# Performance work log

Hardware: AMD Instinct MI355X
Metric: run time of the kernel (lower is better)

Reference implementation:

```python
import jax, jax.numpy as jnp
import numpy as np

N_NODES = 50000

def setup_inputs() -> dict:
    key = jax.random.key(0)
    ks = jax.random.split(key, 8)
    d_in, d_h = 128, 128
    x = jax.random.normal(ks[0], (N_NODES, d_in), dtype=jnp.float32)
    edge_index = jax.random.randint(ks[1], (2, 800000), 0, N_NODES, dtype=jnp.int64)
    edge_pairs = jax.random.randint(ks[2], (1000000, 2), 0, N_NODES, dtype=jnp.int64)
    W_gcn = jax.random.normal(ks[3], (d_in, d_h), dtype=jnp.float32) / np.sqrt(d_in)
    b_gcn = jnp.zeros((d_h,), dtype=jnp.float32)
    W1 = jax.random.normal(ks[4], (2 * d_h, d_h), dtype=jnp.float32) / np.sqrt(2 * d_h)
    b1 = jnp.zeros((d_h,), dtype=jnp.float32)
    W2 = jax.random.normal(ks[5], (d_h, 1), dtype=jnp.float32) / np.sqrt(d_h)
    b2 = jnp.zeros((1,), dtype=jnp.float32)
    return {"x": x, "edge_index": edge_index, "edge_pairs": edge_pairs,
            "W_gcn": W_gcn, "b_gcn": b_gcn, "W1": W1, "b1": b1, "W2": W2, "b2": b2}

def gcn_conv(x, edge_index, W, b):
    # PyG GCNConv default: add self-loops, symmetric normalization.
    n = x.shape[0]
    loop = jnp.arange(n, dtype=edge_index.dtype)
    src = jnp.concatenate([edge_index[0], loop])  # [E+N]
    dst = jnp.concatenate([edge_index[1], loop])
    deg = jax.ops.segment_sum(jnp.ones(src.shape[0], dtype=x.dtype), dst, num_segments=n)
    dinv = jnp.where(deg > 0, jax.lax.rsqrt(deg), 0.0)
    norm = dinv[src] * dinv[dst]                  # [E+N]
    h = x @ W                                     # [N, H]
    agg = jax.ops.segment_sum(h[src] * norm[:, None], dst, num_segments=n)
    return agg + b

def reference(x, edge_index, edge_pairs, W_gcn, b_gcn, W1, b1, W2, b2):
    h = gcn_conv(x, edge_index, W_gcn, b_gcn)      # [N, H]
    e = jnp.concatenate([h[edge_pairs[:, 0]], h[edge_pairs[:, 1]]], axis=-1)  # [P, 2H]
    edge_logits = jax.nn.relu(e @ W1 + b1) @ W2 + b2  # [P, 1]
    return edge_logits, edge_pairs, h
```

## Files before the change

kernel.cpp:

```cpp
#include <hip/hip_runtime.h>
#include <hip/hip_fp16.h>

#define WG 256

typedef _Float16 f16;
typedef _Float16 hv2 __attribute__((ext_vector_type(2)));
typedef _Float16 f16x4 __attribute__((ext_vector_type(4)));
typedef _Float16 f16x8 __attribute__((ext_vector_type(8)));
typedef float f32x4 __attribute__((ext_vector_type(4)));

__global__ __launch_bounds__(WG) void k_deg_count(const int* __restrict__ dst,
                                                  int* __restrict__ deg,
                                                  int* __restrict__ rank, int e) {
    int i = blockIdx.x * WG + threadIdx.x;
    if (i < e) rank[i] = atomicAdd(&deg[dst[i]], 1);
}

__global__ __launch_bounds__(WG) void k_scan1(const int* __restrict__ deg,
                                              float* __restrict__ dinv,
                                              int* __restrict__ base,
                                              int* __restrict__ bsum, int n) {
    __shared__ int t[WG];
    int tid = threadIdx.x;
    int i = blockIdx.x * WG + tid;
    int v = (i < n) ? deg[i] : 0;
    if (i < n) dinv[i] = rsqrtf((float)(v + 1));
    t[tid] = v;
    __syncthreads();
    for (int o = 1; o < WG; o <<= 1) {
        int add = (tid >= o) ? t[tid - o] : 0;
        __syncthreads();
        t[tid] += add;
        __syncthreads();
    }
    if (i < n) base[i] = t[tid] - v;
    if (tid == WG - 1) bsum[blockIdx.x] = t[WG - 1];
}

__global__ __launch_bounds__(WG) void k_scan23(int* __restrict__ base,
                                               const int* __restrict__ bsum,
                                               int n, int e, int nb) {
    __shared__ int t[WG];
    int tid = threadIdx.x;
    int v = (tid < nb) ? bsum[tid] : 0;
    t[tid] = v;
    __syncthreads();
    for (int o = 1; o < WG; o <<= 1) {
        int add = (tid >= o) ? t[tid - o] : 0;
        __syncthreads();
        t[tid] += add;
        __syncthreads();
    }
    int off = t[blockIdx.x] - ((blockIdx.x < nb) ? bsum[blockIdx.x] : 0);
    int i = blockIdx.x * WG + tid;
    if (i < n) {
        base[i] += off;
        if (i == n - 1) base[n] = e;
    }
}

__global__ __launch_bounds__(WG) void k_fill(const int* __restrict__ src,
                                             const int* __restrict__ dst,
                                             const int* __restrict__ base,
                                             const int* __restrict__ rank,
                                             int* __restrict__ esrc, int e) {
    int i = blockIdx.x * WG + threadIdx.x;
    if (i >= e) return;
    esrc[base[dst[i]] + rank[i]] = src[i];
}

__global__ __launch_bounds__(WG) void k_misc(const float* __restrict__ Wg,
                                             f16* __restrict__ Wgt,
                                             const float* __restrict__ W1,
                                             f16* __restrict__ W1t,
                                             const int* __restrict__ pairs,
                                             float* __restrict__ outp, int n4) {
    int b = blockIdx.x;
    if (b < 64) {
        int i = b * WG + threadIdx.x;
        int k = i & 127, nI = i >> 7;
        Wgt[i] = (f16)Wg[(size_t)k * 128 + nI];
    } else if (b < 192) {
        int i = (b - 64) * WG + threadIdx.x;
        int k = i & 255, nI = i >> 8;
        W1t[i] = (f16)W1[(size_t)k * 128 + nI];
    } else {
        int i = (b - 192) * WG + threadIdx.x;
        if (i < n4) {
            int4 v = ((const int4*)pairs)[i];
            ((float4*)outp)[i] = make_float4((float)v.x, (float)v.y, (float)v.z, (float)v.w);
        }
    }
}

__global__ __launch_bounds__(WG) void k_mm_hpk(const float* __restrict__ A,
                                               const f16* __restrict__ Wt,
                                               const float* __restrict__ dinv,
                                               __half2* __restrict__ Out, int n) {
    __shared__ f16 As[64][136];
    __shared__ f16 Bs[128][136];
    const int tid = threadIdx.x;
    const int row0 = blockIdx.x * 64;
    for (int f = tid; f < 128 * 16; f += WG) {
        int r = f >> 4, c = f & 15;
        *(float4*)&Bs[r][c * 8] = ((const float4*)Wt)[r * 16 + c];
    }
    for (int f = tid; f < 64 * 32; f += WG) {
        int r = f >> 5, c = f & 31;
        float4 v = make_float4(0.f, 0.f, 0.f, 0.f);
        if (row0 + r < n) v = ((const float4*)A)[(size_t)(row0 + r) * 32 + c];
        *(f16x4*)&As[r][c * 4] = (f16x4){(f16)v.x, (f16)v.y, (f16)v.z, (f16)v.w};
    }
    __syncthreads();
    const int wv = tid >> 6, lane = tid & 63, m = lane & 15, quad = lane >> 4;
    f32x4 acc[8];
#pragma unroll
    for (int t = 0; t < 8; ++t) acc[t] = (f32x4){0.f, 0.f, 0.f, 0.f};
#pragma unroll
    for (int kk = 0; kk < 4; ++kk) {
        f16x8 af = *(f16x8*)&As[wv * 16 + m][kk * 32 + quad * 8];
#pragma unroll
        for (int t = 0; t < 8; ++t) {
            f16x8 bf = *(f16x8*)&Bs[t * 16 + m][kk * 32 + quad * 8];
            acc[t] = __builtin_amdgcn_mfma_f32_16x16x32_f16(af, bf, acc[t], 0, 0, 0);
        }
    }
#pragma unroll
    for (int r = 0; r < 4; ++r) {
        int row = row0 + wv * 16 + quad * 4 + r;
        if (row < n) {
            float dv = dinv[row];
#pragma unroll
            for (int t = 0; t < 4; ++t)
                Out[(size_t)row * 64 + t * 16 + m] =
                    __floats2half2_rn(acc[t][r] * dv, acc[t + 4][r] * dv);
        }
    }
}

__global__ __launch_bounds__(WG) void k_mm_uv(const float* __restrict__ A,
                                              const f16* __restrict__ W1t,
                                              const float* __restrict__ b1,
                                              __half2* __restrict__ Up,
                                              __half2* __restrict__ Vp, int n) {
    __shared__ f16 As[64][136];
    __shared__ f16 Bs[128][136];
    const int tid = threadIdx.x;
    const int row0 = blockIdx.x * 64;
    for (int f = tid; f < 64 * 32; f += WG) {
        int r = f >> 5, c = f & 31;
        float4 v = make_float4(0.f, 0.f, 0.f, 0.f);
        if (row0 + r < n) v = ((const float4*)A)[(size_t)(row0 + r) * 32 + c];
        *(f16x4*)&As[r][c * 4] = (f16x4){(f16)v.x, (f16)v.y, (f16)v.z, (f16)v.w};
    }
    const int wv = tid >> 6, lane = tid & 63, m = lane & 15, quad = lane >> 4;
    f32x4 acc[8];
#pragma unroll
    for (int ph = 0; ph < 2; ++ph) {
        if (ph) __syncthreads();
        for (int f = tid; f < 128 * 16; f += WG) {
            int r = f >> 4, c = f & 15;
            *(float4*)&Bs[r][c * 8] = *(const float4*)(W1t + (size_t)r * 256 + ph * 128 + c * 8);
        }
        __syncthreads();
#pragma unroll
        for (int t = 0; t < 8; ++t) acc[t] = (f32x4){0.f, 0.f, 0.f, 0.f};
#pragma unroll
        for (int kk = 0; kk < 4; ++kk) {
            f16x8 af = *(f16x8*)&As[wv * 16 + m][kk * 32 + quad * 8];
#pragma unroll
            for (int t = 0; t < 8; ++t) {
                f16x8 bf = *(f16x8*)&Bs[t * 16 + m][kk * 32 + quad * 8];
                acc[t] = __builtin_amdgcn_mfma_f32_16x16x32_f16(af, bf, acc[t], 0, 0, 0);
            }
        }
        __half2* Out = ph ? Vp : Up;
#pragma unroll
        for (int t = 0; t < 4; ++t) {
            float bl = 0.f, bh = 0.f;
            if (!ph) { bl = b1[t * 16 + m]; bh = b1[t * 16 + m + 64]; }
#pragma unroll
            for (int r = 0; r < 4; ++r) {
                int row = row0 + wv * 16 + quad * 4 + r;
                if (row < n)
                    Out[(size_t)row * 64 + t * 16 + m] =
                        __floats2half2_rn(acc[t][r] + bl, acc[t + 4][r] + bh);
            }
        }
    }
}

__global__ __launch_bounds__(WG) void k_gather(const __half2* __restrict__ Hpk,
                                               const float* __restrict__ dinv,
                                               const float* __restrict__ bg,
                                               const int* __restrict__ base,
                                               const int* __restrict__ esrc,
                                               float* __restrict__ outh, int n) {
    int tid = threadIdx.x;
    int node = blockIdx.x * 16 + (tid >> 4);
    int sub = tid & 15;
    if (node >= n) return;
    int4 hh = *(const int4*)(Hpk + (size_t)node * 64 + 4 * sub);
    const int* hp = (const int*)&hh;
    float accl[4], acch[4];
#pragma unroll
    for (int k = 0; k < 4; ++k) {
        hv2 h = __builtin_bit_cast(hv2, hp[k]);
        accl[k] = (float)h[0];
        acch[k] = (float)h[1];
    }
    int j = base[node], jend = base[node + 1];
    for (; j + 4 <= jend; j += 4) {
        int s0 = esrc[j], s1 = esrc[j + 1], s2i = esrc[j + 2], s3 = esrc[j + 3];
        int4 r0 = *(const int4*)(Hpk + (size_t)s0 * 64 + 4 * sub);
        int4 r1 = *(const int4*)(Hpk + (size_t)s1 * 64 + 4 * sub);
        int4 r2 = *(const int4*)(Hpk + (size_t)s2i * 64 + 4 * sub);
        int4 r3 = *(const int4*)(Hpk + (size_t)s3 * 64 + 4 * sub);
        const int* p0 = (const int*)&r0;
        const int* p1 = (const int*)&r1;
        const int* p2 = (const int*)&r2;
        const int* p3 = (const int*)&r3;
#pragma unroll
        for (int k = 0; k < 4; ++k) {
            hv2 h0 = __builtin_bit_cast(hv2, p0[k]);
            hv2 h1 = __builtin_bit_cast(hv2, p1[k]);
            hv2 h2 = __builtin_bit_cast(hv2, p2[k]);
            hv2 h3 = __builtin_bit_cast(hv2, p3[k]);
            accl[k] += (float)h0[0] + (float)h1[0] + (float)h2[0] + (float)h3[0];
            acch[k] += (float)h0[1] + (float)h1[1] + (float)h2[1] + (float)h3[1];
        }
    }
    for (; j < jend; ++j) {
        int s = esrc[j];
        int4 r = *(const int4*)(Hpk + (size_t)s * 64 + 4 * sub);
        const int* pr = (const int*)&r;
#pragma unroll
        for (int k = 0; k < 4; ++k) {
            hv2 h = __builtin_bit_cast(hv2, pr[k]);
            accl[k] += (float)h[0];
            acch[k] += (float)h[1];
        }
    }
    float dv = dinv[node];
    float4 blo = *(const float4*)(bg + 4 * sub);
    float4 bhi = *(const float4*)(bg + 4 * sub + 64);
    *(float4*)&outh[(size_t)node * 128 + 4 * sub] =
        make_float4(fmaf(accl[0], dv, blo.x), fmaf(accl[1], dv, blo.y),
                    fmaf(accl[2], dv, blo.z), fmaf(accl[3], dv, blo.w));
    *(float4*)&outh[(size_t)node * 128 + 64 + 4 * sub] =
        make_float4(fmaf(acch[0], dv, bhi.x), fmaf(acch[1], dv, bhi.y),
                    fmaf(acch[2], dv, bhi.z), fmaf(acch[3], dv, bhi.w));
}

__global__ __launch_bounds__(WG) void k_pair16(const __half2* __restrict__ U,
                                               const __half2* __restrict__ V,
                                               const float* __restrict__ W2,
                                               const float* __restrict__ b2,
                                               const int* __restrict__ pairs,
                                               float* __restrict__ out_logit, int p) {
    int wv = (blockIdx.x * WG + threadIdx.x) >> 6;
    int lane = threadIdx.x & 63;
    int g = lane >> 4, sub = lane & 15;
    int qb = wv * 16 + g;
    if (qb >= p) return;
    int q0 = qb;
    int q1 = (qb + 4 < p) ? qb + 4 : qb;
    int q2 = (qb + 8 < p) ? qb + 8 : qb;
    int q3 = (qb + 12 < p) ? qb + 12 : qb;
    int a0 = pairs[2 * q0], b0 = pairs[2 * q0 + 1];
    int a1 = pairs[2 * q1], b1i = pairs[2 * q1 + 1];
    int a2 = pairs[2 * q2], b2i = pairs[2 * q2 + 1];
    int a3 = pairs[2 * q3], b3i = pairs[2 * q3 + 1];

    int4 u0 = *(const int4*)(U + (size_t)a0 * 64 + 4 * sub);
    int4 v0 = *(const int4*)(V + (size_t)b0 * 64 + 4 * sub);
    int4 u1 = *(const int4*)(U + (size_t)a1 * 64 + 4 * sub);
    int4 v1 = *(const int4*)(V + (size_t)b1i * 64 + 4 * sub);
    int4 u2 = *(const int4*)(U + (size_t)a2 * 64 + 4 * sub);
    int4 v2 = *(const int4*)(V + (size_t)b2i * 64 + 4 * sub);
    int4 u3 = *(const int4*)(U + (size_t)a3 * 64 + 4 * sub);
    int4 v3 = *(const int4*)(V + (size_t)b3i * 64 + 4 * sub);

    float4 w2lo = ((const float4*)W2)[sub];
    float4 w2hi = ((const float4*)(W2 + 64))[sub];
    hv2 w2h[4];
    w2h[0] = hv2{(f16)w2lo.x, (f16)w2hi.x};
    w2h[1] = hv2{(f16)w2lo.y, (f16)w2hi.y};
    w2h[2] = hv2{(f16)w2lo.z, (f16)w2hi.z};
    w2h[3] = hv2{(f16)w2lo.w, (f16)w2hi.w};

    const int* ui0 = (const int*)&u0;
    const int* vi0 = (const int*)&v0;
    const int* ui1 = (const int*)&u1;
    const int* vi1 = (const int*)&v1;
    const int* ui2 = (const int*)&u2;
    const int* vi2 = (const int*)&v2;
    const int* ui3 = (const int*)&u3;
    const int* vi3 = (const int*)&v3;

    const hv2 z2 = hv2{(f16)0.f, (f16)0.f};
    float p0 = 0.f, p1 = 0.f, p2 = 0.f, p3 = 0.f;
#pragma unroll
    for (int k = 0; k < 4; ++k) {
        hv2 s0 = __builtin_bit_cast(hv2, ui0[k]) + __builtin_bit_cast(hv2, vi0[k]);
        hv2 s1 = __builtin_bit_cast(hv2, ui1[k]) + __builtin_bit_cast(hv2, vi1[k]);
        hv2 s2 = __builtin_bit_cast(hv2, ui2[k]) + __builtin_bit_cast(hv2, vi2[k]);
        hv2 s3 = __builtin_bit_cast(hv2, ui3[k]) + __builtin_bit_cast(hv2, vi3[k]);
        p0 = __builtin_amdgcn_fdot2(__builtin_elementwise_max(s0, z2), w2h[k], p0, false);
        p1 = __builtin_amdgcn_fdot2(__builtin_elementwise_max(s1, z2), w2h[k], p1, false);
        p2 = __builtin_amdgcn_fdot2(__builtin_elementwise_max(s2, z2), w2h[k], p2, false);
        p3 = __builtin_amdgcn_fdot2(__builtin_elementwise_max(s3, z2), w2h[k], p3, false);
    }
#pragma unroll
    for (int m = 1; m < 16; m <<= 1) {
        p0 += __shfl_xor(p0, m, 64);
        p1 += __shfl_xor(p1, m, 64);
        p2 += __shfl_xor(p2, m, 64);
        p3 += __shfl_xor(p3, m, 64);
    }
    if (sub == 0) {
        float bb = b2[0];
        out_logit[q0] = p0 + bb;
        if (qb + 4 < p) out_logit[qb + 4] = p1 + bb;
        if (qb + 8 < p) out_logit[qb + 8] = p2 + bb;
        if (qb + 12 < p) out_logit[qb + 12] = p3 + bb;
    }
}

extern "C" void kernel_launch(void* const* d_in, const int* in_sizes, int n_in,
                              void* d_out, int out_size, void* d_ws, size_t ws_size,
                              hipStream_t stream) {
    const float* x     = (const float*)d_in[0];
    const int*   eidx  = (const int*)d_in[1];
    const int*   pairs = (const int*)d_in[2];
    const float* W_gcn = (const float*)d_in[3];
    const float* b_gcn = (const float*)d_in[4];
    const float* W1    = (const float*)d_in[5];
    const float* b1    = (const float*)d_in[6];
    const float* W2    = (const float*)d_in[7];
    const float* b2    = (const float*)d_in[8];

    const int N = in_sizes[0] / 128;
    const int E = in_sizes[1] / 2;
    const int P = in_sizes[2] / 2;
    const int* esrc_in = eidx;
    const int* edst_in = eidx + E;

    float* ws      = (float*)d_ws;
    int*   deg     = (int*)d_ws;
    float* dinv    = ws + 65536;
    int*   base    = (int*)(ws + 131072);
    int*   bsum    = (int*)(ws + 196608);
    f16*   Wt_gcn  = (f16*)(ws + 197120);
    f16*   W1t     = (f16*)(ws + 205312);
    int*   rank    = (int*)(ws + 221696);
    int*   ecsr    = (int*)(ws + 221696 + (size_t)E);
    __half2* Hpk   = (__half2*)(ws + 221696 + 2 * (size_t)E);
    __half2* Upk   = Hpk + (size_t)N * 64;
    __half2* Vpk   = Upk + (size_t)N * 64;

    float* out_logit = (float*)d_out;
    float* out_pairs = out_logit + P;
    float* out_h     = out_logit + 3 * (size_t)P;

    const int nb = (N + WG - 1) / WG;
    dim3 blk(WG);
    dim3 grid_pair((unsigned)((P + 63) / 64));
    dim3 grid_misc((unsigned)(192 + (P / 2 + WG - 1) / WG));
    hipMemsetAsync(deg, 0, (size_t)N * 4, stream);
    k_deg_count <<<(E + WG - 1) / WG, blk, 0, stream>>>(edst_in, deg, rank, E);
    k_scan1     <<<nb, blk, 0, stream>>>(deg, dinv, base, bsum, N);
    k_scan23    <<<nb, blk, 0, stream>>>(base, bsum, N, E, nb);
    k_fill      <<<(E + WG - 1) / WG, blk, 0, stream>>>(esrc_in, edst_in, base, rank, ecsr, E);
    k_misc      <<<grid_misc, blk, 0, stream>>>(W_gcn, Wt_gcn, W1, W1t, pairs, out_pairs, P / 2);
    k_mm_hpk    <<<(N + 63) / 64, blk, 0, stream>>>(x, Wt_gcn, dinv, Hpk, N);
    k_gather    <<<(N + 15) / 16, blk, 0, stream>>>(Hpk, dinv, b_gcn, base, ecsr, out_h, N);
    k_mm_uv     <<<(N + 63) / 64, blk, 0, stream>>>(out_h, W1t, b1, Upk, Vpk, N);
    k_pair16    <<<grid_pair, blk, 0, stream>>>(Upk, Vpk, W2, b2, pairs, out_logit, P);
}
```

Baseline: 276.6 us.

## Fuse degree counting, pair conversion and X@W GEMM into one interleaved launch

The dinv prescale is moved out of the GEMM epilogue and into the gather, where each neighbor's row is scaled by its own dinv through FMAs. The GEMM therefore no longer depends on the degree count. That lets the degree atomics, the pair int-to-float conversion and the X@W GEMM run as interleaved block slots of a single launch. The goal is to overlap the atomic-bound and bandwidth-bound work with the MFMA GEMM and to drop one launch. In exchange, the gather does an extra dinv lookup per edge, and the grid carries idle blocks wherever the slot counts differ.

```diff
diff --git a/kernel.cpp b/kernel.cpp
--- a/kernel.cpp
+++ b/kernel.cpp
@@ -9,11 +9,88 @@
 typedef _Float16 f16x8 __attribute__((ext_vector_type(8)));
 typedef float f32x4 __attribute__((ext_vector_type(4)));
 
-__global__ __launch_bounds__(WG) void k_deg_count(const int* __restrict__ dst,
-                                                  int* __restrict__ deg,
-                                                  int* __restrict__ rank, int e) {
-    int i = blockIdx.x * WG + threadIdx.x;
-    if (i < e) rank[i] = atomicAdd(&deg[dst[i]], 1);
+__global__ __launch_bounds__(WG) void k_misc0(const float* __restrict__ Wg,
+                                              f16* __restrict__ Wgt,
+                                              const float* __restrict__ W1,
+                                              f16* __restrict__ W1t) {
+    int b = blockIdx.x;
+    if (b < 64) {
+        int i = b * WG + threadIdx.x;
+        int k = i & 127, nI = i >> 7;
+        Wgt[i] = (f16)Wg[(size_t)k * 128 + nI];
+    } else {
+        int i = (b - 64) * WG + threadIdx.x;
+        int k = i & 255, nI = i >> 8;
+        W1t[i] = (f16)W1[(size_t)k * 128 + nI];
+    }
+}
+
+__global__ __launch_bounds__(WG) void k_fusedA(const float* __restrict__ A,
+                                               const f16* __restrict__ Wt,
+                                               __half2* __restrict__ Out, int n,
+                                               const int* __restrict__ dst,
+                                               int* __restrict__ deg,
+                                               int* __restrict__ rank, int e,
+                                               const int* __restrict__ pairs,
+                                               float* __restrict__ outp, int n4,
+                                               int nmm, int necnt, int ncvt) {
+    __shared__ __align__(16) char smem[64 * 136 * 2 + 128 * 136 * 2];
+    int b = blockIdx.x, slot = b & 3, idx = b >> 2;
+    int tid = threadIdx.x;
+    if (slot == 1 || slot == 3) {
+        int hid = idx * 2 + (slot >> 1);
+        if (hid >= necnt) return;
+        int i = hid * WG + tid;
+        if (i < e) rank[i] = atomicAdd(&deg[dst[i]], 1);
+        return;
+    }
+    if (slot == 2) {
+        if (idx >= ncvt) return;
+        int i = idx * WG + tid;
+        if (i < n4) {
+            int4 v = ((const int4*)pairs)[i];
+            ((float4*)outp)[i] = make_float4((float)v.x, (float)v.y, (float)v.z, (float)v.w);
+        }
+        return;
+    }
+    if (idx >= nmm) return;
+    f16(*As)[136] = (f16(*)[136])smem;
+    f16(*Bs)[136] = (f16(*)[136])(smem + 64 * 136 * 2);
+    const int row0 = idx * 64;
+    for (int f = tid; f < 128 * 16; f += WG) {
+        int r = f >> 4, c = f & 15;
+        *(float4*)&Bs[r][c * 8] = ((const float4*)Wt)[r * 16 + c];
+    }
+    for (int f = tid; f < 64 * 32; f += WG) {
+        int r = f >> 5, c = f & 31;
+        float4 v = make_float4(0.f, 0.f, 0.f, 0.f);
+        if (row0 + r < n) v = ((const float4*)A)[(size_t)(row0 + r) * 32 + c];
+        *(f16x4*)&As[r][c * 4] = (f16x4){(f16)v.x, (f16)v.y, (f16)v.z, (f16)v.w};
+    }
+    __syncthreads();
+    const int wv = tid >> 6, lane = tid & 63, m = lane & 15, quad = lane >> 4;
+    f32x4 acc[8];
+#pragma unroll
+    for (int t = 0; t < 8; ++t) acc[t] = (f32x4){0.f, 0.f, 0.f, 0.f};
+#pragma unroll
+    for (int kk = 0; kk < 4; ++kk) {
+        f16x8 af = *(f16x8*)&As[wv * 16 + m][kk * 32 + quad * 8];
+#pragma unroll
+        for (int t = 0; t < 8; ++t) {
+            f16x8 bf = *(f16x8*)&Bs[t * 16 + m][kk * 32 + quad * 8];
+            acc[t] = __builtin_amdgcn_mfma_f32_16x16x32_f16(af, bf, acc[t], 0, 0, 0);
+        }
+    }
+#pragma unroll
+    for (int r = 0; r < 4; ++r) {
+        int row = row0 + wv * 16 + quad * 4 + r;
+        if (row < n) {
+#pragma unroll
+            for (int t = 0; t < 4; ++t)
+                Out[(size_t)row * 64 + t * 16 + m] =
+                    __floats2half2_rn(acc[t][r], acc[t + 4][r]);
+        }
+    }
 }
 
 __global__ __launch_bounds__(WG) void k_scan1(const int* __restrict__ deg,
@@ -69,73 +146,74 @@
     esrc[base[dst[i]] + rank[i]] = src[i];
 }
 
-__global__ __launch_bounds__(WG) void k_misc(const float* __restrict__ Wg,
-                                             f16* __restrict__ Wgt,
-                                             const float* __restrict__ W1,
-                                             f16* __restrict__ W1t,
-                                             const int* __restrict__ pairs,
-                                             float* __restrict__ outp, int n4) {
-    int b = blockIdx.x;
-    if (b < 64) {
-        int i = b * WG + threadIdx.x;
-        int k = i & 127, nI = i >> 7;
-        Wgt[i] = (f16)Wg[(size_t)k * 128 + nI];
-    } else if (b < 192) {
-        int i = (b - 64) * WG + threadIdx.x;
-        int k = i & 255, nI = i >> 8;
-        W1t[i] = (f16)W1[(size_t)k * 128 + nI];
-    } else {
-        int i = (b - 192) * WG + threadIdx.x;
-        if (i < n4) {
-            int4 v = ((const int4*)pairs)[i];
-            ((float4*)outp)[i] = make_float4((float)v.x, (float)v.y, (float)v.z, (float)v.w);
-        }
-    }
-}
-
-__global__ __launch_bounds__(WG) void k_mm_hpk(const float* __restrict__ A,
-                                               const f16* __restrict__ Wt,
+__global__ __launch_bounds__(WG) void k_gather(const __half2* __restrict__ Hpk,
                                                const float* __restrict__ dinv,
-                                               __half2* __restrict__ Out, int n) {
-    __shared__ f16 As[64][136];
-    __shared__ f16 Bs[128][136];
-    const int tid = threadIdx.x;
-    const int row0 = blockIdx.x * 64;
-    for (int f = tid; f < 128 * 16; f += WG) {
-        int r = f >> 4, c = f & 15;
-        *(float4*)&Bs[r][c * 8] = ((const float4*)Wt)[r * 16 + c];
-    }
-    for (int f = tid; f < 64 * 32; f += WG) {
-        int r = f >> 5, c = f & 31;
-        float4 v = make_float4(0.f, 0.f, 0.f, 0.f);
-        if (row0 + r < n) v = ((const float4*)A)[(size_t)(row0 + r) * 32 + c];
-        *(f16x4*)&As[r][c * 4] = (f16x4){(f16)v.x, (f16)v.y, (f16)v.z, (f16)v.w};
-    }
-    __syncthreads();
-    const int wv = tid >> 6, lane = tid & 63, m = lane & 15, quad = lane >> 4;
-    f32x4 acc[8];
-#pragma unroll
-    for (int t = 0; t < 8; ++t) acc[t] = (f32x4){0.f, 0.f, 0.f, 0.f};
-#pragma unroll
-    for (int kk = 0; kk < 4; ++kk) {
-        f16x8 af = *(f16x8*)&As[wv * 16 + m][kk * 32 + quad * 8];
-#pragma unroll
-        for (int t = 0; t < 8; ++t) {
-            f16x8 bf = *(f16x8*)&Bs[t * 16 + m][kk * 32 + quad * 8];
-            acc[t] = __builtin_amdgcn_mfma_f32_16x16x32_f16(af, bf, acc[t], 0, 0, 0);
-        }
-    }
-#pragma unroll
-    for (int r = 0; r < 4; ++r) {
-        int row = row0 + wv * 16 + quad * 4 + r;
-        if (row < n) {
-            float dv = dinv[row];
-#pragma unroll
-            for (int t = 0; t < 4; ++t)
-                Out[(size_t)row * 64 + t * 16 + m] =
-                    __floats2half2_rn(acc[t][r] * dv, acc[t + 4][r] * dv);
-        }
-    }
+                                               const float* __restrict__ bg,
+                                               const int* __restrict__ base,
+                                               const int* __restrict__ esrc,
+                                               float* __restrict__ outh, int n) {
+    int tid = threadIdx.x;
+    int node = blockIdx.x * 16 + (tid >> 4);
+    int sub = tid & 15;
+    if (node >= n) return;
+    float dv = dinv[node];
+    int4 hh = *(const int4*)(Hpk + (size_t)node * 64 + 4 * sub);
+    const int* hp = (const int*)&hh;
+    float accl[4], acch[4];
+#pragma unroll
+    for (int k = 0; k < 4; ++k) {
+        hv2 h = __builtin_bit_cast(hv2, hp[k]);
+        accl[k] = (float)h[0] * dv;
+        acch[k] = (float)h[1] * dv;
+    }
+    int j = base[node], jend = base[node + 1];
+    for (; j + 4 <= jend; j += 4) {
+        int s0 = esrc[j], s1 = esrc[j + 1], s2i = esrc[j + 2], s3 = esrc[j + 3];
+        float ds0 = dinv[s0], ds1 = dinv[s1], ds2 = dinv[s2i], ds3 = dinv[s3];
+        int4 r0 = *(const int4*)(Hpk + (size_t)s0 * 64 + 4 * sub);
+        int4 r1 = *(const int4*)(Hpk + (size_t)s1 * 64 + 4 * sub);
+        int4 r2 = *(const int4*)(Hpk + (size_t)s2i * 64 + 4 * sub);
+        int4 r3 = *(const int4*)(Hpk + (size_t)s3 * 64 + 4 * sub);
+        const int* p0 = (const int*)&r0;
+        const int* p1 = (const int*)&r1;
+        const int* p2 = (const int*)&r2;
+        const int* p3 = (const int*)&r3;
+#pragma unroll
+        for (int k = 0; k < 4; ++k) {
+            hv2 h0 = __builtin_bit_cast(hv2, p0[k]);
+            hv2 h1 = __builtin_bit_cast(hv2, p1[k]);
+            hv2 h2 = __builtin_bit_cast(hv2, p2[k]);
+            hv2 h3 = __builtin_bit_cast(hv2, p3[k]);
+            accl[k] = fmaf((float)h0[0], ds0, accl[k]);
+            accl[k] = fmaf((float)h1[0], ds1, accl[k]);
+            accl[k] = fmaf((float)h2[0], ds2, accl[k]);
+            accl[k] = fmaf((float)h3[0], ds3, accl[k]);
+            acch[k] = fmaf((float)h0[1], ds0, acch[k]);
+            acch[k] = fmaf((float)h1[1], ds1, acch[k]);
+            acch[k] = fmaf((float)h2[1], ds2, acch[k]);
+            acch[k] = fmaf((float)h3[1], ds3, acch[k]);
+        }
+    }
+    for (; j < jend; ++j) {
+        int s = esrc[j];
+        float ds = dinv[s];
+        int4 r = *(const int4*)(Hpk + (size_t)s * 64 + 4 * sub);
+        const int* pr = (const int*)&r;
+#pragma unroll
+        for (int k = 0; k < 4; ++k) {
+            hv2 h = __builtin_bit_cast(hv2, pr[k]);
+            accl[k] = fmaf((float)h[0], ds, accl[k]);
+            acch[k] = fmaf((float)h[1], ds, acch[k]);
+        }
+    }
+    float4 blo = *(const float4*)(bg + 4 * sub);
+    float4 bhi = *(const float4*)(bg + 4 * sub + 64);
+    *(float4*)&outh[(size_t)node * 128 + 4 * sub] =
+        make_float4(fmaf(accl[0], dv, blo.x), fmaf(accl[1], dv, blo.y),
+                    fmaf(accl[2], dv, blo.z), fmaf(accl[3], dv, blo.w));
+    *(float4*)&outh[(size_t)node * 128 + 64 + 4 * sub] =
+        make_float4(fmaf(acch[0], dv, bhi.x), fmaf(acch[1], dv, bhi.y),
+                    fmaf(acch[2], dv, bhi.z), fmaf(acch[3], dv, bhi.w));
 }
 
 __global__ __launch_bounds__(WG) void k_mm_uv(const float* __restrict__ A,
@@ -188,68 +266,6 @@
             }
         }
     }
-}
-
-__global__ __launch_bounds__(WG) void k_gather(const __half2* __restrict__ Hpk,
-                                               const float* __restrict__ dinv,
-                                               const float* __restrict__ bg,
-                                               const int* __restrict__ base,
-                                               const int* __restrict__ esrc,
-                                               float* __restrict__ outh, int n) {
-    int tid = threadIdx.x;
-    int node = blockIdx.x * 16 + (tid >> 4);
-    int sub = tid & 15;
-    if (node >= n) return;
-    int4 hh = *(const int4*)(Hpk + (size_t)node * 64 + 4 * sub);
-    const int* hp = (const int*)&hh;
-    float accl[4], acch[4];
-#pragma unroll
-    for (int k = 0; k < 4; ++k) {
-        hv2 h = __builtin_bit_cast(hv2, hp[k]);
-        accl[k] = (float)h[0];
-        acch[k] = (float)h[1];
-    }
-    int j = base[node], jend = base[node + 1];
-    for (; j + 4 <= jend; j += 4) {
-        int s0 = esrc[j], s1 = esrc[j + 1], s2i = esrc[j + 2], s3 = esrc[j + 3];
-        int4 r0 = *(const int4*)(Hpk + (size_t)s0 * 64 + 4 * sub);
-        int4 r1 = *(const int4*)(Hpk + (size_t)s1 * 64 + 4 * sub);
-        int4 r2 = *(const int4*)(Hpk + (size_t)s2i * 64 + 4 * sub);
-        int4 r3 = *(const int4*)(Hpk + (size_t)s3 * 64 + 4 * sub);
-        const int* p0 = (const int*)&r0;
-        const int* p1 = (const int*)&r1;
-        const int* p2 = (const int*)&r2;
-        const int* p3 = (const int*)&r3;
-#pragma unroll
-        for (int k = 0; k < 4; ++k) {
-            hv2 h0 = __builtin_bit_cast(hv2, p0[k]);
-            hv2 h1 = __builtin_bit_cast(hv2, p1[k]);
-            hv2 h2 = __builtin_bit_cast(hv2, p2[k]);
-            hv2 h3 = __builtin_bit_cast(hv2, p3[k]);
-            accl[k] += (float)h0[0] + (float)h1[0] + (float)h2[0] + (float)h3[0];
-            acch[k] += (float)h0[1] + (float)h1[1] + (float)h2[1] + (float)h3[1];
-        }
-    }
-    for (; j < jend; ++j) {
-        int s = esrc[j];
-        int4 r = *(const int4*)(Hpk + (size_t)s * 64 + 4 * sub);
-        const int* pr = (const int*)&r;
-#pragma unroll
-        for (int k = 0; k < 4; ++k) {
-            hv2 h = __builtin_bit_cast(hv2, pr[k]);
-            accl[k] += (float)h[0];
-            acch[k] += (float)h[1];
-        }
-    }
-    float dv = dinv[node];
-    float4 blo = *(const float4*)(bg + 4 * sub);
-    float4 bhi = *(const float4*)(bg + 4 * sub + 64);
-    *(float4*)&outh[(size_t)node * 128 + 4 * sub] =
-        make_float4(fmaf(accl[0], dv, blo.x), fmaf(accl[1], dv, blo.y),
-                    fmaf(accl[2], dv, blo.z), fmaf(accl[3], dv, blo.w));
-    *(float4*)&outh[(size_t)node * 128 + 64 + 4 * sub] =
-        make_float4(fmaf(acch[0], dv, bhi.x), fmaf(acch[1], dv, bhi.y),
-                    fmaf(acch[2], dv, bhi.z), fmaf(acch[3], dv, bhi.w));
 }
 
 __global__ __launch_bounds__(WG) void k_pair16(const __half2* __restrict__ U,
@@ -354,8 +370,8 @@
     f16*   Wt_gcn  = (f16*)(ws + 197120);
     f16*   W1t     = (f16*)(ws + 205312);
     int*   rank    = (int*)(ws + 221696);
-    int*   ecsr    = (int*)(ws + 221696 + (size_t)E);
-    __half2* Hpk   = (__half2*)(ws + 221696 + 2 * (size_t)E);
+    int*   ecsr    = rank + (size_t)E;
+    __half2* Hpk   = (__half2*)(ecsr + (size_t)E);
     __half2* Upk   = Hpk + (size_t)N * 64;
     __half2* Vpk   = Upk + (size_t)N * 64;
 
@@ -363,18 +379,26 @@
     float* out_pairs = out_logit + P;
     float* out_h     = out_logit + 3 * (size_t)P;
 
-    const int nb = (N + WG - 1) / WG;
+    const int nb    = (N + WG - 1) / WG;
+    const int nmm   = (N + 63) / 64;
+    const int necnt = (E + WG - 1) / WG;
+    const int ncvt  = (P / 2 + WG - 1) / WG;
+    int gmax = nmm;
+    int h2 = (necnt + 1) / 2;
+    if (h2 > gmax) gmax = h2;
+    if (ncvt > gmax) gmax = ncvt;
     dim3 blk(WG);
-    dim3 grid_pair((unsigned)((P + 63) / 64));
-    dim3 grid_misc((unsigned)(192 + (P / 2 + WG - 1) / WG));
+
     hipMemsetAsync(deg, 0, (size_t)N * 4, stream);
-    k_deg_count <<<(E + WG - 1) / WG, blk, 0, stream>>>(edst_in, deg, rank, E);
-    k_scan1     <<<nb, blk, 0, stream>>>(deg, dinv, base, bsum, N);
-    k_scan23    <<<nb, blk, 0, stream>>>(base, bsum, N, E, nb);
-    k_fill      <<<(E + WG - 1) / WG, blk, 0, stream>>>(esrc_in, edst_in, base, rank, ecsr, E);
-    k_misc      <<<grid_misc, blk, 0, stream>>>(W_gcn, Wt_gcn, W1, W1t, pairs, out_pairs, P / 2);
-    k_mm_hpk    <<<(N + 63) / 64, blk, 0, stream>>>(x, Wt_gcn, dinv, Hpk, N);
-    k_gather    <<<(N + 15) / 16, blk, 0, stream>>>(Hpk, dinv, b_gcn, base, ecsr, out_h, N);
-    k_mm_uv     <<<(N + 63) / 64, blk, 0, stream>>>(out_h, W1t, b1, Upk, Vpk, N);
-    k_pair16    <<<grid_pair, blk, 0, stream>>>(Upk, Vpk, W2, b2, pairs, out_logit, P);
-}
+    k_misc0  <<<192, blk, 0, stream>>>(W_gcn, Wt_gcn, W1, W1t);
+    k_fusedA <<<4 * gmax, blk, 0, stream>>>(x, Wt_gcn, Hpk, N,
+                                            edst_in, deg, rank, E,
+                                            pairs, out_pairs, P / 2,
+                                            nmm, necnt, ncvt);
+    k_scan1  <<<nb, blk, 0, stream>>>(deg, dinv, base, bsum, N);
+    k_scan23 <<<nb, blk, 0, stream>>>(base, bsum, N, E, nb);
+    k_fill   <<<necnt, blk, 0, stream>>>(esrc_in, edst_in, base, rank, ecsr, E);
+    k_gather <<<(N + 15) / 16, blk, 0, stream>>>(Hpk, dinv, b_gcn, base, ecsr, out_h, N);
+    k_mm_uv  <<<nmm, blk, 0, stream>>>(out_h, W1t, b1, Upk, Vpk, N);
+    k_pair16 <<<(P + 63) / 64, blk, 0, stream>>>(Upk, Vpk, W2, b2, pairs, out_logit, P);
+}
```

Measured after the change: 276.0 us. No clear change (-0.2%).
